# Performance work log

Hardware: AMD Instinct MI355X
Metric: run time of the kernel (lower is better)

## Reference

```python
import jax, jax.numpy as jnp
import numpy as np

HEAD_COUNT = 16
EMBED_DIM = 2048
B, S = 2, 2048


def setup_inputs() -> dict:
    key = jax.random.key(0)
    k1, k2, k3, k4, k5 = jax.random.split(key, 5)
    keys = jax.random.normal(k1, (B, S, EMBED_DIM), dtype=jnp.float32)
    values = jax.random.normal(k2, (B, S, EMBED_DIM), dtype=jnp.float32)
    queries = jax.random.normal(k3, (B, S, EMBED_DIM), dtype=jnp.float32)
    # padding-style mask; guarantee at least one valid key per batch row
    attention_mask = jax.random.randint(k4, (B, S), 0, 2).astype(bool)
    attention_mask = attention_mask.at[:, 0].set(True)
    w_out = jax.random.normal(k5, (EMBED_DIM, EMBED_DIM), dtype=jnp.float32) * (EMBED_DIM ** -0.5)
    return {"keys": keys, "values": values, "queries": queries,
            "attention_mask": attention_mask, "w_out": w_out}


def reference(keys, values, queries, attention_mask, w_out):
    b, s, e = queries.shape
    h = HEAD_COUNT
    c = e // h  # head dim
    k = keys.reshape(b, s, h, c)
    v = values.reshape(b, s, h, c)
    q = queries.reshape(b, s, h, c) * (c ** -0.5)
    # [B,H,Q,K] scores + additive padding bias on key axis
    scores = jnp.einsum('bqhc,bkhc->bhqk', q, k)
    bias = jnp.where(attention_mask, 0.0, -jnp.inf)[:, None, None, :]
    weights = jax.nn.softmax(scores + bias, axis=-1)
    out = jnp.einsum('bhqk,bkhc->bqhc', weights, v).reshape(b, s, e)
    # nn.Linear(bias=False): y = x @ W^T
    return out @ w_out.T
```

## Files before the change

kernel.cpp:

```cpp
#include <hip/hip_runtime.h>
#include <hip/hip_bf16.h>
#include <math.h>

#define B_ 2
#define S_ 2048
#define E_ 2048
#define H_ 16
#define C_ 128

typedef __attribute__((ext_vector_type(8))) short s8v;
typedef __attribute__((ext_vector_type(4))) float f32x4;
typedef __attribute__((ext_vector_type(2))) unsigned u32x2;
typedef __attribute__((ext_vector_type(4))) unsigned u32x4;

#define MFMA16(a, b, c) __builtin_amdgcn_mfma_f32_16x16x32_bf16((a), (b), (c), 0, 0, 0)

__device__ __forceinline__ unsigned fbits(float f) {
    union { float f; unsigned u; } v{f};
    return v.u;
}
__device__ __forceinline__ short f2bfh(float f) {
    return (short)((fbits(f) + 0x8000u) >> 16);
}
__device__ __forceinline__ unsigned bfpack(float lo, float hi) {
    return __builtin_amdgcn_perm(fbits(hi) + 0x8000u, fbits(lo) + 0x8000u, 0x07060302u);
}

__device__ __forceinline__ void glds16(const void* g, void* l) {
    __builtin_amdgcn_global_load_lds(
        (const __attribute__((address_space(1))) void*)g,
        (__attribute__((address_space(3))) void*)l, 16, 0, 0);
}

template <bool DOK>
__global__ __launch_bounds__(256) void prep_kv(
    const float* __restrict__ K, const float* __restrict__ V,
    short* __restrict__ Kb, short* __restrict__ Vt)
{
    __shared__ __align__(16) short vt[C_][66];
    const int t  = threadIdx.x;
    const int s0 = blockIdx.x * 64;
    const int bh = blockIdx.y;
    const int b = bh >> 4, h = bh & 15;

    if (DOK) {
#pragma unroll
        for (int i = 0; i < 8; ++i) {
            int idx = t + i * 256;
            int s = idx >> 5, c4 = idx & 31;
            float4 v = *(const float4*)(K + ((size_t)(b * S_ + s0 + s)) * E_ + h * C_ + c4 * 4);
            u32x2 o = {bfpack(v.x, v.y), bfpack(v.z, v.w)};
            *(u32x2*)(Kb + ((size_t)(bh * S_ + s0 + s)) * C_ + c4 * 4) = o;
        }
    }
#pragma unroll
    for (int i = 0; i < 8; ++i) {
        int idx = t + i * 256;
        int r = idx >> 5, c4 = idx & 31;
        float4 v = *(const float4*)(V + ((size_t)(b * S_ + s0 + r)) * E_ + h * C_ + c4 * 4);
        vt[c4 * 4 + 0][r] = f2bfh(v.x);
        vt[c4 * 4 + 1][r] = f2bfh(v.y);
        vt[c4 * 4 + 2][r] = f2bfh(v.z);
        vt[c4 * 4 + 3][r] = f2bfh(v.w);
    }
    __syncthreads();
#pragma unroll
    for (int i = 0; i < 4; ++i) {
        int idx = t + i * 256;
        int c = idx >> 3, sc = idx & 7;
        *(s8v*)(Vt + ((size_t)(bh * C_ + c)) * S_ + s0 + sc * 8) = *(const s8v*)&vt[c][sc * 8];
    }
}

__global__ __launch_bounds__(256) void convw_kernel(
    const float* __restrict__ W, short* __restrict__ Wb)
{
    size_t i = ((size_t)blockIdx.x * 256 + threadIdx.x) * 8;
    float4 a = *(const float4*)(W + i);
    float4 b = *(const float4*)(W + i + 4);
    u32x4 o = {bfpack(a.x, a.y), bfpack(a.z, a.w), bfpack(b.x, b.y), bfpack(b.z, b.w)};
    *(u32x4*)(Wb + i) = o;
}

constexpr int QT = 128;
constexpr int KT = 64;
constexpr float M0 = 16.0f;

template <bool KBF16>
__global__ __launch_bounds__(256, 2) void attn_mfma(
    const short* __restrict__ Kb, const float* __restrict__ Kf,
    const float* __restrict__ Qp, const short* __restrict__ Vt,
    const int* __restrict__ maskp, short* __restrict__ Op)
{
    __shared__ __align__(16) short ks[KT * 128];
    __shared__ __align__(16) short vs[C_ * 64];
    __shared__ __align__(16) short ps[4][32][72];
    __shared__ float bias[KT];

    const int t = threadIdx.x;
    const int w = t >> 6, lane = t & 63;
    const int c15 = lane & 15, quad = lane >> 4;
    const int q0 = blockIdx.x * QT;
    const int h = blockIdx.y, b = blockIdx.z;
    const int bh = b * H_ + h;

    const float qscale = 0.12751744458187936f;
    s8v qf[2][4];
#pragma unroll
    for (int mi = 0; mi < 2; ++mi) {
        const float* qrow = Qp + ((size_t)(b * S_ + q0 + w * 32 + mi * 16 + c15)) * E_ + h * C_;
#pragma unroll
        for (int kk = 0; kk < 4; ++kk) {
            const float* p = qrow + kk * 32 + quad * 8;
            float4 x0 = *(const float4*)p;
            float4 x1 = *(const float4*)(p + 4);
            u32x4 pk = {bfpack(x0.x * qscale, x0.y * qscale),
                        bfpack(x0.z * qscale, x0.w * qscale),
                        bfpack(x1.x * qscale, x1.y * qscale),
                        bfpack(x1.z * qscale, x1.w * qscale)};
            qf[mi][kk] = *(s8v*)&pk;
        }
    }

    s8v ones;
#pragma unroll
    for (int j = 0; j < 8; ++j) ones[j] = (short)0x3F80;

    f32x4 O[2][8], Ol[2];
#pragma unroll
    for (int mi = 0; mi < 2; ++mi) {
        Ol[mi] = (f32x4){0.f, 0.f, 0.f, 0.f};
#pragma unroll
        for (int ct = 0; ct < 8; ++ct) O[mi][ct] = (f32x4){0.f, 0.f, 0.f, 0.f};
    }

    const short* Kbh = Kb + (size_t)(bh * S_) * C_;
    const float* Kfh = Kf + (size_t)(b * S_) * E_ + h * C_;
    const short* Vbh = Vt + (size_t)(bh * C_) * S_;
    const int*   mbase = maskp + b * S_;

    int kgp[4], vgp[2];
#pragma unroll
    for (int kk = 0; kk < 4; ++kk) kgp[kk] = ((4 * kk + quad) ^ c15) * 8;
#pragma unroll
    for (int ks2 = 0; ks2 < 2; ++ks2) vgp[ks2] = ((4 * ks2 + quad) ^ (c15 & 7)) * 8;

    for (int k0 = 0; k0 < S_; k0 += KT) {
        if (KBF16) {
            const int r4 = lane >> 4, gp = lane & 15;
#pragma unroll
            for (int i = 0; i < 4; ++i) {
                int row = w * 16 + i * 4 + r4;
                int g = gp ^ ((row >> 2) & 15);
                glds16(Kbh + (size_t)(k0 + row) * C_ + g * 8, &ks[(w * 16 + i * 4) * 128]);
            }
        } else {
#pragma unroll
            for (int i = 0; i < 8; ++i) {
                int idx = t + i * 256;
                int r = idx >> 5, c4 = idx & 31;
                float4 kv = *(const float4*)(Kfh + (size_t)(k0 + r) * E_ + c4 * 4);
                u32x2 sv = {bfpack(kv.x, kv.y), bfpack(kv.z, kv.w)};
                int gpw = (c4 >> 1) ^ ((r >> 2) & 15);
                *(u32x2*)&ks[r * 128 + gpw * 8 + (c4 & 1) * 4] = sv;
            }
        }
        {
            const int cr = lane >> 3, gp = lane & 7;
#pragma unroll
            for (int i = 0; i < 4; ++i) {
                int c = w * 32 + i * 8 + cr;
                int g = gp ^ (c & 7);
                glds16(Vbh + (size_t)c * S_ + k0 + g * 8, &vs[(w * 32 + i * 8) * 64]);
            }
        }
        if (t < KT) bias[t] = mbase[k0 + t] ? -M0 : -1e30f;
        __syncthreads();

        float4 bvv = *(const float4*)&bias[4 * c15];
        float bva[4] = {bvv.x, bvv.y, bvv.z, bvv.w};
        f32x4 Sf[2][4];
#pragma unroll
        for (int nt = 0; nt < 4; ++nt) {
            f32x4 s0 = (f32x4){bva[nt], bva[nt], bva[nt], bva[nt]};
            f32x4 s1 = s0;
            const short* krow = &ks[(4 * c15 + nt) * 128];
#pragma unroll
            for (int kk = 0; kk < 4; ++kk) {
                s8v bf = *(const s8v*)(krow + kgp[kk]);
                s0 = MFMA16(qf[0][kk], bf, s0);
                s1 = MFMA16(qf[1][kk], bf, s1);
            }
            Sf[0][nt] = s0; Sf[1][nt] = s1;
        }

#pragma unroll
        for (int mi = 0; mi < 2; ++mi)
#pragma unroll
            for (int r = 0; r < 4; ++r) {
                float p0 = exp2f(Sf[mi][0][r]);
                float p1 = exp2f(Sf[mi][1][r]);
                float p2 = exp2f(Sf[mi][2][r]);
                float p3 = exp2f(Sf[mi][3][r]);
                u32x2 d = {bfpack(p0, p1), bfpack(p2, p3)};
                *(u32x2*)&ps[w][mi * 16 + quad * 4 + r][4 * c15] = d;
            }

        s8v af[2][2];
#pragma unroll
        for (int mi = 0; mi < 2; ++mi)
#pragma unroll
            for (int ks2 = 0; ks2 < 2; ++ks2)
                af[mi][ks2] = *(const s8v*)&ps[w][mi * 16 + c15][ks2 * 32 + quad * 8];
#pragma unroll
        for (int ct = 0; ct < 8; ++ct) {
            const short* vrow = &vs[(ct * 16 + c15) * 64];
#pragma unroll
            for (int ks2 = 0; ks2 < 2; ++ks2) {
                s8v bf = *(const s8v*)(vrow + vgp[ks2]);
                O[0][ct] = MFMA16(af[0][ks2], bf, O[0][ct]);
                O[1][ct] = MFMA16(af[1][ks2], bf, O[1][ct]);
            }
        }
#pragma unroll
        for (int mi = 0; mi < 2; ++mi) {
            Ol[mi] = MFMA16(af[mi][0], ones, Ol[mi]);
            Ol[mi] = MFMA16(af[mi][1], ones, Ol[mi]);
        }
        __syncthreads();
    }

#pragma unroll
    for (int mi = 0; mi < 2; ++mi) {
        float inv[4];
#pragma unroll
        for (int r = 0; r < 4; ++r) inv[r] = 1.f / Ol[mi][r];
        size_t rbase = (size_t)(b * S_ + q0 + w * 32 + mi * 16 + quad * 4) * E_ + h * C_;
#pragma unroll
        for (int ct = 0; ct < 8; ++ct)
#pragma unroll
            for (int r = 0; r < 4; ++r)
                Op[rbase + (size_t)r * E_ + ct * 16 + c15] = f2bfh(O[mi][ct][r] * inv[r]);
    }
}

template <bool WBF16>
__global__ __launch_bounds__(256, 2) void proj_mfma(
    const short* __restrict__ X, const short* __restrict__ Wb,
    const float* __restrict__ Wf, float* __restrict__ Y)
{
    __shared__ __align__(16) short As[128 * 64];
    __shared__ __align__(16) short Bs[128 * 64];

    const int t = threadIdx.x;
    const int w = t >> 6, lane = t & 63;
    const int c15 = lane & 15, quad = lane >> 4;
    const int bm = blockIdx.x * 128, bn = blockIdx.y * 128;
    const int wm = (w >> 1) * 64, wn = (w & 1) * 64;

    f32x4 acc[4][4];
#pragma unroll
    for (int mi = 0; mi < 4; ++mi)
#pragma unroll
        for (int ni = 0; ni < 4; ++ni) acc[mi][ni] = (f32x4){0.f, 0.f, 0.f, 0.f};

    int agp[2];
#pragma unroll
    for (int kk = 0; kk < 2; ++kk) agp[kk] = ((4 * kk + quad) ^ (c15 & 7)) * 8;

    for (int k0 = 0; k0 < E_; k0 += 64) {
        {
            const int r8 = lane >> 3, gp = lane & 7;
#pragma unroll
            for (int i = 0; i < 4; ++i) {
                int row = w * 32 + i * 8 + r8;
                int g = gp ^ (row & 7);
                glds16(X + (size_t)(bm + row) * E_ + k0 + g * 8, &As[(w * 32 + i * 8) * 64]);
                if (WBF16)
                    glds16(Wb + (size_t)(bn + row) * E_ + k0 + g * 8, &Bs[(w * 32 + i * 8) * 64]);
            }
        }
        if (!WBF16) {
#pragma unroll
            for (int i = 0; i < 8; ++i) {
                int idx = t + i * 256;
                int r = idx >> 4, c4 = idx & 15;
                float4 wv = *(const float4*)(Wf + (size_t)(bn + r) * E_ + k0 + c4 * 4);
                u32x2 sv = {bfpack(wv.x, wv.y), bfpack(wv.z, wv.w)};
                int gpw = (c4 >> 1) ^ (r & 7);
                *(u32x2*)&Bs[r * 64 + gpw * 8 + (c4 & 1) * 4] = sv;
            }
        }
        __syncthreads();

#pragma unroll
        for (int kk = 0; kk < 2; ++kk) {
            s8v a[4], bb[4];
#pragma unroll
            for (int mi = 0; mi < 4; ++mi)
                a[mi] = *(const s8v*)&As[(wm + mi * 16 + c15) * 64 + agp[kk]];
#pragma unroll
            for (int ni = 0; ni < 4; ++ni)
                bb[ni] = *(const s8v*)&Bs[(wn + ni * 16 + c15) * 64 + agp[kk]];
#pragma unroll
            for (int mi = 0; mi < 4; ++mi)
#pragma unroll
                for (int ni = 0; ni < 4; ++ni)
                    acc[mi][ni] = MFMA16(a[mi], bb[ni], acc[mi][ni]);
        }
        __syncthreads();
    }

#pragma unroll
    for (int mi = 0; mi < 4; ++mi)
#pragma unroll
        for (int ni = 0; ni < 4; ++ni) {
            size_t rbase = (size_t)(bm + wm + mi * 16 + quad * 4) * E_ + bn + wn + ni * 16 + c15;
#pragma unroll
            for (int r = 0; r < 4; ++r) Y[rbase + (size_t)r * E_] = acc[mi][ni][r];
        }
}

extern "C" void kernel_launch(void* const* d_in, const int* in_sizes, int n_in,
                              void* d_out, int out_size, void* d_ws, size_t ws_size,
                              hipStream_t stream) {
    const float* keys    = (const float*)d_in[0];
    const float* values  = (const float*)d_in[1];
    const float* queries = (const float*)d_in[2];
    const int*   mask    = (const int*)d_in[3];
    const float* w_out   = (const float*)d_in[4];
    float* out = (float*)d_out;

    const size_t EL = (size_t)B_ * S_ * E_;
    short* ws  = (short*)d_ws;
    short* VtW = ws;
    short* Xb  = ws + EL;
    short* Kb  = ws + 2 * EL;
    short* Wb  = ws + 3 * EL;

    const bool hasK = ws_size >= (3 * EL) * 2;
    const bool hasW = ws_size >= (3 * EL + (size_t)E_ * E_) * 2;

    if (hasK)
        prep_kv<true><<<dim3(S_ / 64, B_ * H_), 256, 0, stream>>>(keys, values, Kb, VtW);
    else
        prep_kv<false><<<dim3(S_ / 64, B_ * H_), 256, 0, stream>>>(keys, values, Kb, VtW);
    if (hasW) convw_kernel<<<(E_ * E_ / 8) / 256, 256, 0, stream>>>(w_out, Wb);

    if (hasK)
        attn_mfma<true><<<dim3(S_ / QT, H_, B_), 256, 0, stream>>>(Kb, keys, queries, VtW, mask, Xb);
    else
        attn_mfma<false><<<dim3(S_ / QT, H_, B_), 256, 0, stream>>>(Kb, keys, queries, VtW, mask, Xb);

    if (hasW)
        proj_mfma<true><<<dim3((B_ * S_) / 128, E_ / 128), 256, 0, stream>>>(Xb, Wb, w_out, out);
    else
        proj_mfma<false><<<dim3((B_ * S_) / 128, E_ / 128), 256, 0, stream>>>(Xb, Wb, w_out, out);
}
```

Baseline: 279.9 us.

## Double-buffer K/V and GEMM tiles in LDS to overlap loads with MFMA

Both the attention kernel and the projection GEMM now use two LDS buffers, so the async global-to-LDS copy for the next tile is issued before computing on the current one, with one barrier per tile. The attention kernel also reads mask values straight from global memory into registers instead of through an LDS bias array, shrinks the P scratch buffer to per-mi reuse, and raises wave priority around MFMA sections. The goal is to hide global load latency. In exchange LDS use roughly doubles, which may limit occupancy at the declared two blocks per SM.

```diff
diff --git a/kernel.cpp b/kernel.cpp
--- a/kernel.cpp
+++ b/kernel.cpp
@@ -92,10 +92,9 @@
     const float* __restrict__ Qp, const short* __restrict__ Vt,
     const int* __restrict__ maskp, short* __restrict__ Op)
 {
-    __shared__ __align__(16) short ks[KT * 128];
-    __shared__ __align__(16) short vs[C_ * 64];
-    __shared__ __align__(16) short ps[4][32][72];
-    __shared__ float bias[KT];
+    __shared__ __align__(16) short ks[2][KT * 128];
+    __shared__ __align__(16) short vs[2][C_ * 64];
+    __shared__ __align__(16) short ps[4][16][72];
 
     const int t = threadIdx.x;
     const int w = t >> 6, lane = t & 63;
@@ -137,7 +136,7 @@
     const short* Kbh = Kb + (size_t)(bh * S_) * C_;
     const float* Kfh = Kf + (size_t)(b * S_) * E_ + h * C_;
     const short* Vbh = Vt + (size_t)(bh * C_) * S_;
-    const int*   mbase = maskp + b * S_;
+    const int*   mptr = maskp + b * S_ + 4 * c15;
 
     int kgp[4], vgp[2];
 #pragma unroll
@@ -145,16 +144,102 @@
 #pragma unroll
     for (int ks2 = 0; ks2 < 2; ++ks2) vgp[ks2] = ((4 * ks2 + quad) ^ (c15 & 7)) * 8;
 
-    for (int k0 = 0; k0 < S_; k0 += KT) {
-        if (KBF16) {
-            const int r4 = lane >> 4, gp = lane & 15;
-#pragma unroll
-            for (int i = 0; i < 4; ++i) {
-                int row = w * 16 + i * 4 + r4;
-                int g = gp ^ ((row >> 2) & 15);
-                glds16(Kbh + (size_t)(k0 + row) * C_ + g * 8, &ks[(w * 16 + i * 4) * 128]);
-            }
-        } else {
+    auto stage = [&](short* ksb, short* vsb, int k0) {
+        const int r4 = lane >> 4, gp = lane & 15;
+#pragma unroll
+        for (int i = 0; i < 4; ++i) {
+            int row = w * 16 + i * 4 + r4;
+            int g = gp ^ ((row >> 2) & 15);
+            glds16(Kbh + (size_t)(k0 + row) * C_ + g * 8, ksb + (w * 16 + i * 4) * 128);
+        }
+        const int cr = lane >> 3, gp7 = lane & 7;
+#pragma unroll
+        for (int i = 0; i < 4; ++i) {
+            int c = w * 32 + i * 8 + cr;
+            int g = gp7 ^ (c & 7);
+            glds16(Vbh + (size_t)c * S_ + k0 + g * 8, vsb + (w * 32 + i * 8) * 64);
+        }
+    };
+
+    auto compute = [&](const short* ksc, const short* vsc, int4 mv) {
+        float bva[4] = {mv.x ? -M0 : -1e30f, mv.y ? -M0 : -1e30f,
+                        mv.z ? -M0 : -1e30f, mv.w ? -M0 : -1e30f};
+        f32x4 Sf[2][4];
+        __builtin_amdgcn_s_setprio(1);
+#pragma unroll
+        for (int nt = 0; nt < 4; ++nt) {
+            f32x4 s0 = (f32x4){bva[nt], bva[nt], bva[nt], bva[nt]};
+            f32x4 s1 = s0;
+            const short* krow = ksc + (4 * c15 + nt) * 128;
+#pragma unroll
+            for (int kk = 0; kk < 4; ++kk) {
+                s8v bf = *(const s8v*)(krow + kgp[kk]);
+                s0 = MFMA16(qf[0][kk], bf, s0);
+                s1 = MFMA16(qf[1][kk], bf, s1);
+            }
+            Sf[0][nt] = s0; Sf[1][nt] = s1;
+        }
+        __builtin_amdgcn_s_setprio(0);
+
+        s8v af[2][2];
+#pragma unroll
+        for (int mi = 0; mi < 2; ++mi) {
+#pragma unroll
+            for (int r = 0; r < 4; ++r) {
+                float p0 = exp2f(Sf[mi][0][r]);
+                float p1 = exp2f(Sf[mi][1][r]);
+                float p2 = exp2f(Sf[mi][2][r]);
+                float p3 = exp2f(Sf[mi][3][r]);
+                u32x2 d = {bfpack(p0, p1), bfpack(p2, p3)};
+                *(u32x2*)&ps[w][quad * 4 + r][4 * c15] = d;
+            }
+#pragma unroll
+            for (int ks2 = 0; ks2 < 2; ++ks2)
+                af[mi][ks2] = *(const s8v*)&ps[w][c15][ks2 * 32 + quad * 8];
+        }
+
+        __builtin_amdgcn_s_setprio(1);
+#pragma unroll
+        for (int ct = 0; ct < 8; ++ct) {
+            const short* vrow = vsc + (ct * 16 + c15) * 64;
+#pragma unroll
+            for (int ks2 = 0; ks2 < 2; ++ks2) {
+                s8v bf = *(const s8v*)(vrow + vgp[ks2]);
+                O[0][ct] = MFMA16(af[0][ks2], bf, O[0][ct]);
+                O[1][ct] = MFMA16(af[1][ks2], bf, O[1][ct]);
+            }
+        }
+#pragma unroll
+        for (int mi = 0; mi < 2; ++mi) {
+            Ol[mi] = MFMA16(af[mi][0], ones, Ol[mi]);
+            Ol[mi] = MFMA16(af[mi][1], ones, Ol[mi]);
+        }
+        __builtin_amdgcn_s_setprio(0);
+    };
+
+    if (KBF16) {
+        stage(&ks[0][0], &vs[0][0], 0);
+        int4 mcur = *(const int4*)mptr;
+        __syncthreads();
+#pragma unroll 1
+        for (int k0 = 0; k0 < S_; k0 += 2 * KT) {
+            stage(&ks[1][0], &vs[1][0], k0 + KT);
+            int4 m1 = *(const int4*)(mptr + k0 + KT);
+            compute(&ks[0][0], &vs[0][0], mcur);
+            __syncthreads();
+
+            int4 m2 = m1;
+            if (k0 + 2 * KT < S_) {
+                stage(&ks[0][0], &vs[0][0], k0 + 2 * KT);
+                m2 = *(const int4*)(mptr + k0 + 2 * KT);
+            }
+            compute(&ks[1][0], &vs[1][0], m1);
+            mcur = m2;
+            __syncthreads();
+        }
+    } else {
+#pragma unroll 1
+        for (int k0 = 0; k0 < S_; k0 += KT) {
 #pragma unroll
             for (int i = 0; i < 8; ++i) {
                 int idx = t + i * 256;
@@ -162,72 +247,22 @@
                 float4 kv = *(const float4*)(Kfh + (size_t)(k0 + r) * E_ + c4 * 4);
                 u32x2 sv = {bfpack(kv.x, kv.y), bfpack(kv.z, kv.w)};
                 int gpw = (c4 >> 1) ^ ((r >> 2) & 15);
-                *(u32x2*)&ks[r * 128 + gpw * 8 + (c4 & 1) * 4] = sv;
-            }
-        }
-        {
-            const int cr = lane >> 3, gp = lane & 7;
-#pragma unroll
-            for (int i = 0; i < 4; ++i) {
-                int c = w * 32 + i * 8 + cr;
-                int g = gp ^ (c & 7);
-                glds16(Vbh + (size_t)c * S_ + k0 + g * 8, &vs[(w * 32 + i * 8) * 64]);
-            }
-        }
-        if (t < KT) bias[t] = mbase[k0 + t] ? -M0 : -1e30f;
-        __syncthreads();
-
-        float4 bvv = *(const float4*)&bias[4 * c15];
-        float bva[4] = {bvv.x, bvv.y, bvv.z, bvv.w};
-        f32x4 Sf[2][4];
-#pragma unroll
-        for (int nt = 0; nt < 4; ++nt) {
-            f32x4 s0 = (f32x4){bva[nt], bva[nt], bva[nt], bva[nt]};
-            f32x4 s1 = s0;
-            const short* krow = &ks[(4 * c15 + nt) * 128];
-#pragma unroll
-            for (int kk = 0; kk < 4; ++kk) {
-                s8v bf = *(const s8v*)(krow + kgp[kk]);
-                s0 = MFMA16(qf[0][kk], bf, s0);
-                s1 = MFMA16(qf[1][kk], bf, s1);
-            }
-            Sf[0][nt] = s0; Sf[1][nt] = s1;
-        }
-
-#pragma unroll
-        for (int mi = 0; mi < 2; ++mi)
-#pragma unroll
-            for (int r = 0; r < 4; ++r) {
-                float p0 = exp2f(Sf[mi][0][r]);
-                float p1 = exp2f(Sf[mi][1][r]);
-                float p2 = exp2f(Sf[mi][2][r]);
-                float p3 = exp2f(Sf[mi][3][r]);
-                u32x2 d = {bfpack(p0, p1), bfpack(p2, p3)};
-                *(u32x2*)&ps[w][mi * 16 + quad * 4 + r][4 * c15] = d;
-            }
-
-        s8v af[2][2];
-#pragma unroll
-        for (int mi = 0; mi < 2; ++mi)
-#pragma unroll
-            for (int ks2 = 0; ks2 < 2; ++ks2)
-                af[mi][ks2] = *(const s8v*)&ps[w][mi * 16 + c15][ks2 * 32 + quad * 8];
-#pragma unroll
-        for (int ct = 0; ct < 8; ++ct) {
-            const short* vrow = &vs[(ct * 16 + c15) * 64];
-#pragma unroll
-            for (int ks2 = 0; ks2 < 2; ++ks2) {
-                s8v bf = *(const s8v*)(vrow + vgp[ks2]);
-                O[0][ct] = MFMA16(af[0][ks2], bf, O[0][ct]);
-                O[1][ct] = MFMA16(af[1][ks2], bf, O[1][ct]);
-            }
-        }
-#pragma unroll
-        for (int mi = 0; mi < 2; ++mi) {
-            Ol[mi] = MFMA16(af[mi][0], ones, Ol[mi]);
-            Ol[mi] = MFMA16(af[mi][1], ones, Ol[mi]);
-        }
-        __syncthreads();
+                *(u32x2*)&ks[0][r * 128 + gpw * 8 + (c4 & 1) * 4] = sv;
+            }
+            {
+                const int cr = lane >> 3, gp7 = lane & 7;
+#pragma unroll
+                for (int i = 0; i < 4; ++i) {
+                    int c = w * 32 + i * 8 + cr;
+                    int g = gp7 ^ (c & 7);
+                    glds16(Vbh + (size_t)c * S_ + k0 + g * 8, &vs[0][(w * 32 + i * 8) * 64]);
+                }
+            }
+            int4 mv = *(const int4*)(mptr + k0);
+            __syncthreads();
+            compute(&ks[0][0], &vs[0][0], mv);
+            __syncthreads();
+        }
     }
 
 #pragma unroll
@@ -249,8 +284,8 @@
     const short* __restrict__ X, const short* __restrict__ Wb,
     const float* __restrict__ Wf, float* __restrict__ Y)
 {
-    __shared__ __align__(16) short As[128 * 64];
-    __shared__ __align__(16) short Bs[128 * 64];
+    __shared__ __align__(16) short As[2][128 * 64];
+    __shared__ __align__(16) short Bs[2][128 * 64];
 
     const int t = threadIdx.x;
     const int w = t >> 6, lane = t & 63;
@@ -268,19 +303,60 @@
 #pragma unroll
     for (int kk = 0; kk < 2; ++kk) agp[kk] = ((4 * kk + quad) ^ (c15 & 7)) * 8;
 
-    for (int k0 = 0; k0 < E_; k0 += 64) {
-        {
-            const int r8 = lane >> 3, gp = lane & 7;
-#pragma unroll
-            for (int i = 0; i < 4; ++i) {
-                int row = w * 32 + i * 8 + r8;
-                int g = gp ^ (row & 7);
-                glds16(X + (size_t)(bm + row) * E_ + k0 + g * 8, &As[(w * 32 + i * 8) * 64]);
-                if (WBF16)
-                    glds16(Wb + (size_t)(bn + row) * E_ + k0 + g * 8, &Bs[(w * 32 + i * 8) * 64]);
-            }
-        }
-        if (!WBF16) {
+    auto stageAB = [&](short* Ab, short* Bb, int k0) {
+        const int r8 = lane >> 3, gp = lane & 7;
+#pragma unroll
+        for (int i = 0; i < 4; ++i) {
+            int row = w * 32 + i * 8 + r8;
+            int g = gp ^ (row & 7);
+            glds16(X + (size_t)(bm + row) * E_ + k0 + g * 8, Ab + (w * 32 + i * 8) * 64);
+            glds16(Wb + (size_t)(bn + row) * E_ + k0 + g * 8, Bb + (w * 32 + i * 8) * 64);
+        }
+    };
+
+    auto compute = [&](const short* Ab, const short* Bb) {
+#pragma unroll
+        for (int kk = 0; kk < 2; ++kk) {
+            s8v a[4], bb[4];
+#pragma unroll
+            for (int mi = 0; mi < 4; ++mi)
+                a[mi] = *(const s8v*)(Ab + (wm + mi * 16 + c15) * 64 + agp[kk]);
+#pragma unroll
+            for (int ni = 0; ni < 4; ++ni)
+                bb[ni] = *(const s8v*)(Bb + (wn + ni * 16 + c15) * 64 + agp[kk]);
+#pragma unroll
+            for (int mi = 0; mi < 4; ++mi)
+#pragma unroll
+                for (int ni = 0; ni < 4; ++ni)
+                    acc[mi][ni] = MFMA16(a[mi], bb[ni], acc[mi][ni]);
+        }
+    };
+
+    if (WBF16) {
+        stageAB(&As[0][0], &Bs[0][0], 0);
+        __syncthreads();
+#pragma unroll 1
+        for (int k0 = 0; k0 < E_; k0 += 128) {
+            stageAB(&As[1][0], &Bs[1][0], k0 + 64);
+            compute(&As[0][0], &Bs[0][0]);
+            __syncthreads();
+
+            if (k0 + 128 < E_) stageAB(&As[0][0], &Bs[0][0], k0 + 128);
+            compute(&As[1][0], &Bs[1][0]);
+            __syncthreads();
+        }
+    } else {
+#pragma unroll 1
+        for (int k0 = 0; k0 < E_; k0 += 64) {
+            {
+                const int r8 = lane >> 3, gp = lane & 7;
+#pragma unroll
+                for (int i = 0; i < 4; ++i) {
+                    int row = w * 32 + i * 8 + r8;
+                    int g = gp ^ (row & 7);
+                    glds16(X + (size_t)(bm + row) * E_ + k0 + g * 8, &As[0][(w * 32 + i * 8) * 64]);
+                }
+            }
 #pragma unroll
             for (int i = 0; i < 8; ++i) {
                 int idx = t + i * 256;
@@ -288,27 +364,12 @@
                 float4 wv = *(const float4*)(Wf + (size_t)(bn + r) * E_ + k0 + c4 * 4);
                 u32x2 sv = {bfpack(wv.x, wv.y), bfpack(wv.z, wv.w)};
                 int gpw = (c4 >> 1) ^ (r & 7);
-                *(u32x2*)&Bs[r * 64 + gpw * 8 + (c4 & 1) * 4] = sv;
-            }
-        }
-        __syncthreads();
-
-#pragma unroll
-        for (int kk = 0; kk < 2; ++kk) {
-            s8v a[4], bb[4];
-#pragma unroll
-            for (int mi = 0; mi < 4; ++mi)
-                a[mi] = *(const s8v*)&As[(wm + mi * 16 + c15) * 64 + agp[kk]];
-#pragma unroll
-            for (int ni = 0; ni < 4; ++ni)
-                bb[ni] = *(const s8v*)&Bs[(wn + ni * 16 + c15) * 64 + agp[kk]];
-#pragma unroll
-            for (int mi = 0; mi < 4; ++mi)
-#pragma unroll
-                for (int ni = 0; ni < 4; ++ni)
-                    acc[mi][ni] = MFMA16(a[mi], bb[ni], acc[mi][ni]);
-        }
-        __syncthreads();
+                *(u32x2*)&Bs[0][r * 64 + gpw * 8 + (c4 & 1) * 4] = sv;
+            }
+            __syncthreads();
+            compute(&As[0][0], &Bs[0][0]);
+            __syncthreads();
+        }
     }
 
 #pragma unroll
```

Result: no change. 281.6 us (+0.6%).
